# Kernel optimization log

Measured on AMD Instinct MI355X. Metric: run time of the kernel, lower is better.

The kernel has to match this reference:

```python
import jax, jax.numpy as jnp
import numpy as np


def _forgetting_attn(q, k, v, g):
    # q, k, v: [B, T, H, D]; g: [B, T, H] per-step log decay (log-space)
    scale = q.shape[-1] ** -0.5
    scores = jnp.einsum('bqhd,bkhd->bhqk', q, k) * scale  # [B,H,T,T]
    gc = jnp.cumsum(g, axis=1).transpose(0, 2, 1)  # [B,H,T]
    scores = scores + gc[:, :, :, None] - gc[:, :, None, :]
    T = q.shape[1]
    causal = jnp.tril(jnp.ones((T, T), dtype=bool))
    scores = jnp.where(causal, scores, -jnp.inf)
    probs = jax.nn.softmax(scores.astype(jnp.float32), axis=-1).astype(q.dtype)
    return jnp.einsum('bhqk,bkhd->bqhd', probs, v)  # [B,T,H,D]


def setup_inputs() -> dict:
    key = jax.random.key(0)
    ks = jax.random.split(key, 7)
    B, T, H = 1, 2048, 1024
    nh = 16
    s = 0.02
    return {
        'hidden_states': jax.random.normal(ks[0], (B, T, H), jnp.float32),
        'Wq': jax.random.normal(ks[1], (H, H), jnp.float32) * s,
        'Wk': jax.random.normal(ks[2], (H, H), jnp.float32) * s,
        'Wv': jax.random.normal(ks[3], (H, H), jnp.float32) * s,
        'Wf': jax.random.normal(ks[4], (nh, H), jnp.float32) * s,
        'bf': jnp.zeros((nh,), jnp.float32),
        'Wo': jax.random.normal(ks[5], (H, 2 * H), jnp.float32) * s,
    }


def reference(hidden_states, Wq, Wk, Wv, Wf, bf, Wo):
    B, T, H = hidden_states.shape
    nh = Wf.shape[0]
    d = H // nh
    q = (hidden_states @ Wq.T).reshape(B, T, nh, d)
    k = (hidden_states @ Wk.T).reshape(B, T, nh, d)
    v = (hidden_states @ Wv.T).reshape(B, T, nh, d)
    f = jax.nn.log_sigmoid((hidden_states @ Wf.T + bf).astype(jnp.float32))  # [B,T,nh]
    o_fwd = _forgetting_attn(q, k, v, f)
    flip = lambda x: jnp.flip(x, axis=1)
    o_bwd = flip(_forgetting_attn(flip(q), flip(k), flip(v), flip(f)))
    o = jnp.concatenate([o_fwd.reshape(B, T, H), o_bwd.reshape(B, T, H)], axis=-1)
    return o @ Wo.T
```

## Files before the change

kernel.cpp:

```cpp
#include <hip/hip_runtime.h>
#include <math.h>

#define T_SEQ 2048
#define HID   1024
#define NH    16
#define HD    64
#define NT    (T_SEQ / 64)

typedef __attribute__((ext_vector_type(8))) __bf16 bf16x8;
typedef __attribute__((ext_vector_type(4))) float  f32x4;
typedef __attribute__((ext_vector_type(8))) unsigned short u16x8;

#define GPTR(p) (const __attribute__((address_space(1))) void*)(p)
#define SPTR(p) (__attribute__((address_space(3))) void*)(p)

__device__ __forceinline__ unsigned short f2bf(float x) {
    unsigned u = __float_as_uint(x);
    u = (u + 0x7FFF + ((u >> 16) & 1)) >> 16;
    return (unsigned short)u;
}
__device__ __forceinline__ float bf2f(unsigned short u) {
    return __uint_as_float((unsigned)u << 16);
}

__global__ __launch_bounds__(256) void prep1(
    const float* __restrict__ hs,
    const float* __restrict__ Wq, const float* __restrict__ Wk,
    const float* __restrict__ Wv, const float* __restrict__ Wo,
    const float* __restrict__ Wf, const float* __restrict__ bfv,
    unsigned short* __restrict__ hsb, unsigned short* __restrict__ wqb,
    unsigned short* __restrict__ wkb, unsigned short* __restrict__ wvb,
    unsigned short* __restrict__ wob, float* __restrict__ f)
{
    const int y = blockIdx.y;
    if (y < 5) {
        const float* in; unsigned short* out; int n;
        switch (y) {
            case 0: in = hs; out = hsb; n = T_SEQ * HID; break;
            case 1: in = Wq; out = wqb; n = HID * HID;   break;
            case 2: in = Wk; out = wkb; n = HID * HID;   break;
            case 3: in = Wv; out = wvb; n = HID * HID;   break;
            default: in = Wo; out = wob; n = HID * 2 * HID; break;
        }
        const int stride = gridDim.x * blockDim.x;
        for (int i = blockIdx.x * blockDim.x + threadIdx.x; i < n / 4; i += stride) {
            float4 v = reinterpret_cast<const float4*>(in)[i];
            ushort4 r;
            r.x = f2bf(v.x); r.y = f2bf(v.y); r.z = f2bf(v.z); r.w = f2bf(v.w);
            reinterpret_cast<ushort4*>(out)[i] = r;
        }
    } else {
        const int t  = blockIdx.x;
        const int h  = threadIdx.x >> 4;
        const int sl = threadIdx.x & 15;
        const float4* hrow = reinterpret_cast<const float4*>(hs + (size_t)t * HID);
        const float4* wrow = reinterpret_cast<const float4*>(Wf + (size_t)h * HID);
        float s = 0.f;
        #pragma unroll
        for (int i = 0; i < 16; ++i) {
            float4 a = hrow[sl + i * 16];
            float4 b = wrow[sl + i * 16];
            s += a.x * b.x + a.y * b.y + a.z * b.z + a.w * b.w;
        }
        s += __shfl_xor(s, 1);
        s += __shfl_xor(s, 2);
        s += __shfl_xor(s, 4);
        s += __shfl_xor(s, 8);
        if (sl == 0) {
            float x = s + bfv[h];
            f[t * NH + h] = (x >= 0.f) ? -log1pf(expf(-x)) : (x - log1pf(expf(x)));
        }
    }
}

template<int FR>
__device__ __forceinline__ void stage_tile(const unsigned short* __restrict__ G, int K,
                                           int k0, unsigned short* lds, int tid, int w)
{
    #pragma unroll
    for (int j = 0; j < FR; ++j) {
        const int idxb = j * 4096 + tid * 16;
        const int row  = idxb >> 7;
        const int kbyt = idxb & 127;
        const int col  = (kbyt ^ ((row & 7) << 4)) >> 1;
        const int ldsh = (j * 4096 + w * 1024) >> 1;
        __builtin_amdgcn_global_load_lds(
            GPTR(G + (size_t)row * K + k0 + col), SPTR(lds + ldsh), 16, 0, 0);
    }
}

template<int BM, int BN, int EMODE>
__global__ __launch_bounds__(256) void gemm_mfma_bt(
    const unsigned short* __restrict__ A,
    const unsigned short* __restrict__ W0, const unsigned short* __restrict__ W1,
    const unsigned short* __restrict__ W2,
    float* __restrict__ C,
    unsigned short* __restrict__ qb, unsigned short* __restrict__ kb,
    unsigned short* __restrict__ vt,
    int M, int N, int K)
{
    const unsigned short* W = blockIdx.z == 0 ? W0 : (blockIdx.z == 1 ? W1 : W2);

    __shared__ unsigned short Als[2][BM * 64];
    __shared__ unsigned short Bls[2][BN * 64];

    const int gx  = gridDim.x;
    const int nwg = gx * gridDim.y;
    const int lin = blockIdx.y * gx + blockIdx.x;
    const int cpx = nwg >> 3;
    const int sw  = (lin & 7) * cpx + (lin >> 3);
    const int bx  = sw % gx;
    const int by  = sw / gx;

    const int tid = threadIdx.x;
    const int w   = tid >> 6;
    const int l   = tid & 63;
    const int bm  = by * BM;
    const int bn  = bx * BN;
    const int wm  = (w >> 1) * (BM / 2);
    const int wn  = (w & 1) * (BN / 2);
    constexpr int FM = BM / 32;
    constexpr int FN = BN / 32;

    f32x4 acc[FM][FN];
    #pragma unroll
    for (int m = 0; m < FM; ++m)
        #pragma unroll
        for (int n = 0; n < FN; ++n) acc[m][n] = (f32x4){0.f, 0.f, 0.f, 0.f};

    const int frow = l & 15;
    const int kgrp = (l >> 4) * 16;
    const int swz  = (l & 7) << 4;

    const unsigned short* Ag = A + (size_t)bm * K;
    const unsigned short* Wg = W + (size_t)bn * K;

    const int NIT = K >> 6;
    stage_tile<FM>(Ag, K, 0, Als[0], tid, w);
    stage_tile<FN>(Wg, K, 0, Bls[0], tid, w);
    __syncthreads();

    int cur = 0;
    for (int it = 0; it < NIT; ++it) {
        if (it + 1 < NIT) {
            stage_tile<FM>(Ag, K, (it + 1) * 64, Als[cur ^ 1], tid, w);
            stage_tile<FN>(Wg, K, (it + 1) * 64, Bls[cur ^ 1], tid, w);
        }
        const unsigned short* Ap = Als[cur];
        const unsigned short* Bp = Bls[cur];
        #pragma unroll
        for (int ks = 0; ks < 2; ++ks) {
            bf16x8 af[FM], bfr[FN];
            #pragma unroll
            for (int m = 0; m < FM; ++m) {
                const int off = (wm + m * 16 + frow) * 128 + ((ks * 64 + kgrp) ^ swz);
                af[m] = *reinterpret_cast<const bf16x8*>((const char*)Ap + off);
            }
            #pragma unroll
            for (int n = 0; n < FN; ++n) {
                const int off = (wn + n * 16 + frow) * 128 + ((ks * 64 + kgrp) ^ swz);
                bfr[n] = *reinterpret_cast<const bf16x8*>((const char*)Bp + off);
            }
            #pragma unroll
            for (int m = 0; m < FM; ++m)
                #pragma unroll
                for (int n = 0; n < FN; ++n)
                    acc[m][n] = __builtin_amdgcn_mfma_f32_16x16x32_bf16(
                        af[m], bfr[n], acc[m][n], 0, 0, 0);
        }
        __syncthreads();
        cur ^= 1;
    }

    const int r0 = (l >> 4) * 4;
    const int cc = l & 15;
    if (EMODE == 1) {
        #pragma unroll
        for (int m = 0; m < FM; ++m)
            #pragma unroll
            for (int n = 0; n < FN; ++n) {
                float* cp = C + (size_t)(bm + wm + m * 16 + r0) * N + bn + wn + n * 16 + cc;
                #pragma unroll
                for (int r = 0; r < 4; ++r) cp[(size_t)r * N] = acc[m][n][r];
            }
    } else {
        const int z = blockIdx.z;
        if (z == 0) {
            #pragma unroll
            for (int m = 0; m < FM; ++m) {
                const int t0 = bm + wm + m * 16 + r0;
                #pragma unroll
                for (int n = 0; n < FN; ++n) {
                    const int col = bn + wn + n * 16 + cc;
                    #pragma unroll
                    for (int r = 0; r < 4; ++r)
                        qb[(size_t)(t0 + r) * HID + col] = f2bf(acc[m][n][r] * 0.125f);
                }
            }
        } else if (z == 1) {
            #pragma unroll
            for (int m = 0; m < FM; ++m) {
                const int t0 = bm + wm + m * 16 + r0;
                #pragma unroll
                for (int n = 0; n < FN; ++n) {
                    const int col = bn + wn + n * 16 + cc;
                    const int hh  = col >> 6;
                    const int d   = col & 63;
                    #pragma unroll
                    for (int r = 0; r < 4; ++r)
                        kb[(size_t)hh * T_SEQ * HD + (size_t)(t0 + r) * HD + d] =
                            f2bf(acc[m][n][r]);
                }
            }
        } else {
            #pragma unroll
            for (int m = 0; m < FM; ++m) {
                const int t0 = bm + wm + m * 16 + r0;
                #pragma unroll
                for (int n = 0; n < FN; ++n) {
                    const int col = bn + wn + n * 16 + cc;
                    const int hh  = col >> 6;
                    const int d   = col & 63;
                    ushort4 pk;
                    pk.x = f2bf(acc[m][n][0]); pk.y = f2bf(acc[m][n][1]);
                    pk.z = f2bf(acc[m][n][2]); pk.w = f2bf(acc[m][n][3]);
                    *reinterpret_cast<ushort4*>(
                        vt + (size_t)hh * HD * T_SEQ + (size_t)d * T_SEQ + t0) = pk;
                }
            }
        }
    }
}

__global__ __launch_bounds__(256) void prep2(const float* __restrict__ f,
                                             float* __restrict__ gcf,
                                             float* __restrict__ gcb,
                                             const unsigned short* __restrict__ kb,
                                             float* __restrict__ knmax)
{
    const int bid = blockIdx.x;
    if (bid < 32) {
        const int h   = bid >> 1;
        const int rev = bid & 1;
        float* out = rev ? gcb : gcf;
        const int wv   = threadIdx.x >> 6;
        const int lane = threadIdx.x & 63;
        __shared__ float wtot[4];
        float vals[8];
        float run = 0.f;
        #pragma unroll
        for (int c = 0; c < 8; ++c) {
            const int p = wv * 512 + c * 64 + lane;
            const int t = rev ? (T_SEQ - 1 - p) : p;
            float x = f[t * NH + h];
            #pragma unroll
            for (int off = 1; off < 64; off <<= 1) {
                float y = __shfl_up(x, off);
                if (lane >= off) x += y;
            }
            vals[c] = run + x;
            run += __shfl(x, 63);
        }
        if (lane == 0) wtot[wv] = run;
        __syncthreads();
        float prefix = 0.f;
        #pragma unroll
        for (int i = 0; i < 4; ++i) prefix += (i < wv) ? wtot[i] : 0.f;
        #pragma unroll
        for (int c = 0; c < 8; ++c) {
            const int p = wv * 512 + c * 64 + lane;
            const int t = rev ? (T_SEQ - 1 - p) : p;
            out[t * NH + h] = vals[c] + prefix;
        }
    } else {
        const int h    = bid - 32;
        const int tid  = threadIdx.x;
        const int wv   = tid >> 6;
        const int lane = tid & 63;
        __shared__ float wmax[4];
        float mx = 0.f;
        for (int t = tid; t < T_SEQ; t += 256) {
            const u16x8* kr = reinterpret_cast<const u16x8*>(
                kb + (size_t)h * T_SEQ * HD + (size_t)t * HD);
            float s = 0.f;
            #pragma unroll
            for (int i = 0; i < 8; ++i) {
                u16x8 v8 = kr[i];
                #pragma unroll
                for (int j = 0; j < 8; ++j) { float x = bf2f(v8[j]); s += x * x; }
            }
            mx = fmaxf(mx, s);
        }
        #pragma unroll
        for (int off = 32; off > 0; off >>= 1) mx = fmaxf(mx, __shfl_xor(mx, off));
        if (lane == 0) wmax[wv] = mx;
        __syncthreads();
        if (tid == 0) {
            float m = fmaxf(fmaxf(wmax[0], wmax[1]), fmaxf(wmax[2], wmax[3]));
            knmax[h] = sqrtf(m);
        }
    }
}

__global__ __launch_bounds__(256) void attn_flash(
    const unsigned short* __restrict__ qb, const unsigned short* __restrict__ kg,
    const unsigned short* __restrict__ vg,
    const float* __restrict__ gcf, const float* __restrict__ gcb,
    const float* __restrict__ knmax,
    unsigned short* __restrict__ ocat)
{
    const int dir = blockIdx.z;
    const float* gc = dir ? gcb : gcf;
    const int h   = blockIdx.y;
    const int qt  = blockIdx.x;
    const int q0  = qt * 64;
    const int tid = threadIdx.x;
    const int w   = tid >> 6;
    const int l   = tid & 63;
    const int lm  = l & 15;
    const int lg  = l >> 4;
    const int swz = (l & 7) << 4;

    __shared__ unsigned short Kls[64 * 64];
    __shared__ unsigned short Vls[64 * 64];
    __shared__ unsigned short Pls[64 * 64];
    __shared__ float gks[64];
    __shared__ float qbs[64];

    const size_t kgbase = (size_t)h * T_SEQ * HD;
    const size_t vgbase = (size_t)h * HD * T_SEQ;

    const int qrow_a = q0 + 16 * w + lm;
    bf16x8 aq[2];
    aq[0] = *reinterpret_cast<const bf16x8*>(qb + (size_t)qrow_a * HID + h * HD + lg * 8);
    aq[1] = *reinterpret_cast<const bf16x8*>(qb + (size_t)qrow_a * HID + h * HD + 32 + lg * 8);
    float qn2 = 0.f;
    #pragma unroll
    for (int ks = 0; ks < 2; ++ks) {
        u16x8 uv = *reinterpret_cast<const u16x8*>(&aq[ks]);
        #pragma unroll
        for (int j = 0; j < 8; ++j) { float x = bf2f(uv[j]); qn2 += x * x; }
    }
    qn2 += __shfl_xor(qn2, 16);
    qn2 += __shfl_xor(qn2, 32);
    if (lg == 0) qbs[16 * w + lm] = sqrtf(qn2) * knmax[h];

    float gq_r[4];
    #pragma unroll
    for (int reg = 0; reg < 4; ++reg)
        gq_r[reg] = gc[(q0 + 16 * w + lg * 4 + reg) * NH + h];

    float mrun[4], lrun[4];
    #pragma unroll
    for (int reg = 0; reg < 4; ++reg) { mrun[reg] = -1e30f; lrun[reg] = 0.f; }
    f32x4 acc[4];
    #pragma unroll
    for (int db = 0; db < 4; ++db) acc[db] = (f32x4){0.f, 0.f, 0.f, 0.f};

    const int stp = dir ? 1 : -1;
    for (int kt = qt; kt >= 0 && kt < NT; kt += stp) {
        const int k0 = kt * 64;

        #pragma unroll
        for (int j = 0; j < 2; ++j) {
            const int idxb = j * 4096 + tid * 16;
            const int row  = idxb >> 7;
            const int kbyt = idxb & 127;
            const int scol = (kbyt ^ ((row & 7) << 4)) >> 1;
            const int ldsh = (j * 4096 + w * 1024) >> 1;
            __builtin_amdgcn_global_load_lds(
                GPTR(kg + kgbase + (size_t)(k0 + row) * HD + scol),
                SPTR(Kls + ldsh), 16, 0, 0);
            __builtin_amdgcn_global_load_lds(
                GPTR(vg + vgbase + (size_t)row * T_SEQ + k0 + scol),
                SPTR(Vls + ldsh), 16, 0, 0);
        }
        if (w == 0)
            __builtin_amdgcn_global_load_lds(
                GPTR(gc + (size_t)(k0 + l) * NH + h), SPTR(gks), 4, 0, 0);
        __syncthreads();

        f32x4 s[4];
        #pragma unroll
        for (int cb = 0; cb < 4; ++cb) {
            bf16x8 b0 = *reinterpret_cast<const bf16x8*>(
                (char*)Kls + (cb * 16 + lm) * 128 + ((lg * 16) ^ swz));
            bf16x8 b1 = *reinterpret_cast<const bf16x8*>(
                (char*)Kls + (cb * 16 + lm) * 128 + ((64 + lg * 16) ^ swz));
            f32x4 z = (f32x4){0.f, 0.f, 0.f, 0.f};
            z = __builtin_amdgcn_mfma_f32_16x16x32_bf16(aq[0], b0, z, 0, 0, 0);
            s[cb] = __builtin_amdgcn_mfma_f32_16x16x32_bf16(aq[1], b1, z, 0, 0, 0);
        }

        float gk_c[4];
        #pragma unroll
        for (int cb = 0; cb < 4; ++cb) gk_c[cb] = gks[cb * 16 + lm];
        float sv[4][4];
        const bool diag = (kt == qt);
        #pragma unroll
        for (int cb = 0; cb < 4; ++cb)
            #pragma unroll
            for (int reg = 0; reg < 4; ++reg) {
                float x = s[cb][reg] + gq_r[reg] - gk_c[cb];
                if (diag) {
                    const int c_loc = cb * 16 + lm;
                    const int r_loc = 16 * w + lg * 4 + reg;
                    const bool valid = dir ? (c_loc >= r_loc) : (c_loc <= r_loc);
                    x = valid ? x : -1e30f;
                }
                sv[cb][reg] = x;
            }

        float corr[4], mnew[4];
        #pragma unroll
        for (int reg = 0; reg < 4; ++reg) {
            float rm = fmaxf(fmaxf(sv[0][reg], sv[1][reg]), fmaxf(sv[2][reg], sv[3][reg]));
            rm = fmaxf(rm, __shfl_xor(rm, 1));
            rm = fmaxf(rm, __shfl_xor(rm, 2));
            rm = fmaxf(rm, __shfl_xor(rm, 4));
            rm = fmaxf(rm, __shfl_xor(rm, 8));
            mnew[reg] = fmaxf(mrun[reg], rm);
            corr[reg] = __expf(mrun[reg] - mnew[reg]);
            mrun[reg] = mnew[reg];
        }
        float psum[4] = {0.f, 0.f, 0.f, 0.f};
        #pragma unroll
        for (int cb = 0; cb < 4; ++cb)
            #pragma unroll
            for (int reg = 0; reg < 4; ++reg) {
                const float p = __expf(sv[cb][reg] - mnew[reg]);
                psum[reg] += p;
                const int r_loc = 16 * w + lg * 4 + reg;
                *reinterpret_cast<unsigned short*>(
                    (char*)Pls + r_loc * 128 + ((cb * 32 + lm * 2) ^ ((r_loc & 7) << 4))) = f2bf(p);
            }
        #pragma unroll
        for (int reg = 0; reg < 4; ++reg) {
            float ps = psum[reg];
            ps += __shfl_xor(ps, 1);
            ps += __shfl_xor(ps, 2);
            ps += __shfl_xor(ps, 4);
            ps += __shfl_xor(ps, 8);
            lrun[reg] = lrun[reg] * corr[reg] + ps;
        }
        #pragma unroll
        for (int db = 0; db < 4; ++db)
            #pragma unroll
            for (int reg = 0; reg < 4; ++reg) acc[db][reg] *= corr[reg];

        bf16x8 ap[2];
        #pragma unroll
        for (int ks = 0; ks < 2; ++ks)
            ap[ks] = *reinterpret_cast<const bf16x8*>(
                (char*)Pls + (16 * w + lm) * 128 + ((ks * 64 + lg * 16) ^ swz));
        #pragma unroll
        for (int db = 0; db < 4; ++db) {
            bf16x8 bv0 = *reinterpret_cast<const bf16x8*>(
                (char*)Vls + (db * 16 + lm) * 128 + ((lg * 16) ^ swz));
            bf16x8 bv1 = *reinterpret_cast<const bf16x8*>(
                (char*)Vls + (db * 16 + lm) * 128 + ((64 + lg * 16) ^ swz));
            acc[db] = __builtin_amdgcn_mfma_f32_16x16x32_bf16(ap[0], bv0, acc[db], 0, 0, 0);
            acc[db] = __builtin_amdgcn_mfma_f32_16x16x32_bf16(ap[1], bv1, acc[db], 0, 0, 0);
        }

        const int nkt = kt + stp;
        if (nkt >= 0 && nkt < NT) {
            const float gkedge = dir ? gc[(nkt * 64) * NH + h]
                                     : gc[(nkt * 64 + 63) * NH + h];
            int pred = 0;
            #pragma unroll
            for (int reg = 0; reg < 4; ++reg) {
                const float qbv = qbs[16 * w + lg * 4 + reg];
                pred |= (qbv + gq_r[reg] - gkedge) >= (mrun[reg] - 15.f);
            }
            if (!__syncthreads_or(pred)) break;
        }
    }

    float inv[4];
    #pragma unroll
    for (int reg = 0; reg < 4; ++reg) inv[reg] = 1.f / lrun[reg];
    #pragma unroll
    for (int db = 0; db < 4; ++db)
        #pragma unroll
        for (int reg = 0; reg < 4; ++reg) {
            const int row = q0 + 16 * w + lg * 4 + reg;
            const int col = db * 16 + lm;
            ocat[(size_t)row * (2 * HID) + dir * HID + h * HD + col] =
                f2bf(acc[db][reg] * inv[reg]);
        }
}

extern "C" void kernel_launch(void* const* d_in, const int* in_sizes, int n_in,
                              void* d_out, int out_size, void* d_ws, size_t ws_size,
                              hipStream_t stream)
{
    (void)in_sizes; (void)n_in; (void)out_size; (void)ws_size;
    const float* hs = (const float*)d_in[0];
    const float* Wq = (const float*)d_in[1];
    const float* Wk = (const float*)d_in[2];
    const float* Wv = (const float*)d_in[3];
    const float* Wf = (const float*)d_in[4];
    const float* bf = (const float*)d_in[5];
    const float* Wo = (const float*)d_in[6];
    float* out = (float*)d_out;

    float* ws    = (float*)d_ws;
    float* f     = ws;
    float* gcf   = f   + (size_t)T_SEQ * NH;
    float* gcb   = gcf + (size_t)T_SEQ * NH;
    float* knmax = gcb + (size_t)T_SEQ * NH;
    unsigned short* hsb  = (unsigned short*)(knmax + 64);
    unsigned short* wqb  = hsb + (size_t)T_SEQ * HID;
    unsigned short* wkb  = wqb + (size_t)HID * HID;
    unsigned short* wvb  = wkb + (size_t)HID * HID;
    unsigned short* wob  = wvb + (size_t)HID * HID;
    unsigned short* qb   = wob + (size_t)HID * 2 * HID;
    unsigned short* kb   = qb  + (size_t)T_SEQ * HID;
    unsigned short* vt   = kb  + (size_t)T_SEQ * HID;
    unsigned short* ocat = vt  + (size_t)T_SEQ * HID;

    prep1<<<dim3(2048, 6), 256, 0, stream>>>(
        hs, Wq, Wk, Wv, Wo, Wf, bf, hsb, wqb, wkb, wvb, wob, f);

    gemm_mfma_bt<128, 64, 0><<<dim3(HID / 64, T_SEQ / 128, 3), 256, 0, stream>>>(
        hsb, wqb, wkb, wvb, nullptr, qb, kb, vt, T_SEQ, HID, HID);

    prep2<<<48, 256, 0, stream>>>(f, gcf, gcb, kb, knmax);

    attn_flash<<<dim3(NT, NH, 2), 256, 0, stream>>>(qb, kb, vt, gcf, gcb, knmax, ocat);

    gemm_mfma_bt<64, 64, 1><<<dim3(HID / 64, T_SEQ / 64, 1), 256, 0, stream>>>(
        ocat, wob, nullptr, nullptr, out, nullptr, nullptr, nullptr,
        T_SEQ, HID, 2 * HID);
}
```

Baseline: 93.35 us.

## Load K/V tiles directly from global memory and use per-wave early exit

```diff
diff --git a/kernel.cpp b/kernel.cpp
--- a/kernel.cpp
+++ b/kernel.cpp
@@ -101,6 +101,9 @@
 {
     const unsigned short* W = blockIdx.z == 0 ? W0 : (blockIdx.z == 1 ? W1 : W2);
 
+    constexpr int FM = BM / 32;
+    constexpr int FN = BN / 32;
+
     __shared__ unsigned short Als[2][BM * 64];
     __shared__ unsigned short Bls[2][BN * 64];
 
@@ -119,8 +122,6 @@
     const int bn  = bx * BN;
     const int wm  = (w >> 1) * (BM / 2);
     const int wn  = (w & 1) * (BN / 2);
-    constexpr int FM = BM / 32;
-    constexpr int FN = BN / 32;
 
     f32x4 acc[FM][FN];
     #pragma unroll
@@ -321,14 +322,11 @@
     const int lg  = l >> 4;
     const int swz = (l & 7) << 4;
 
-    __shared__ unsigned short Kls[64 * 64];
-    __shared__ unsigned short Vls[64 * 64];
     __shared__ unsigned short Pls[64 * 64];
-    __shared__ float gks[64];
     __shared__ float qbs[64];
 
-    const size_t kgbase = (size_t)h * T_SEQ * HD;
-    const size_t vgbase = (size_t)h * HD * T_SEQ;
+    const unsigned short* kh = kg + (size_t)h * T_SEQ * HD;
+    const unsigned short* vh = vg + (size_t)h * HD * T_SEQ;
 
     const int qrow_a = q0 + 16 * w + lm;
     bf16x8 aq[2];
@@ -361,32 +359,12 @@
     for (int kt = qt; kt >= 0 && kt < NT; kt += stp) {
         const int k0 = kt * 64;
 
-        #pragma unroll
-        for (int j = 0; j < 2; ++j) {
-            const int idxb = j * 4096 + tid * 16;
-            const int row  = idxb >> 7;
-            const int kbyt = idxb & 127;
-            const int scol = (kbyt ^ ((row & 7) << 4)) >> 1;
-            const int ldsh = (j * 4096 + w * 1024) >> 1;
-            __builtin_amdgcn_global_load_lds(
-                GPTR(kg + kgbase + (size_t)(k0 + row) * HD + scol),
-                SPTR(Kls + ldsh), 16, 0, 0);
-            __builtin_amdgcn_global_load_lds(
-                GPTR(vg + vgbase + (size_t)row * T_SEQ + k0 + scol),
-                SPTR(Vls + ldsh), 16, 0, 0);
-        }
-        if (w == 0)
-            __builtin_amdgcn_global_load_lds(
-                GPTR(gc + (size_t)(k0 + l) * NH + h), SPTR(gks), 4, 0, 0);
-        __syncthreads();
-
         f32x4 s[4];
         #pragma unroll
         for (int cb = 0; cb < 4; ++cb) {
-            bf16x8 b0 = *reinterpret_cast<const bf16x8*>(
-                (char*)Kls + (cb * 16 + lm) * 128 + ((lg * 16) ^ swz));
-            bf16x8 b1 = *reinterpret_cast<const bf16x8*>(
-                (char*)Kls + (cb * 16 + lm) * 128 + ((64 + lg * 16) ^ swz));
+            const unsigned short* kr = kh + (size_t)(k0 + cb * 16 + lm) * HD + lg * 8;
+            bf16x8 b0 = *reinterpret_cast<const bf16x8*>(kr);
+            bf16x8 b1 = *reinterpret_cast<const bf16x8*>(kr + 32);
             f32x4 z = (f32x4){0.f, 0.f, 0.f, 0.f};
             z = __builtin_amdgcn_mfma_f32_16x16x32_bf16(aq[0], b0, z, 0, 0, 0);
             s[cb] = __builtin_amdgcn_mfma_f32_16x16x32_bf16(aq[1], b1, z, 0, 0, 0);
@@ -394,7 +372,7 @@
 
         float gk_c[4];
         #pragma unroll
-        for (int cb = 0; cb < 4; ++cb) gk_c[cb] = gks[cb * 16 + lm];
+        for (int cb = 0; cb < 4; ++cb) gk_c[cb] = gc[(k0 + cb * 16 + lm) * NH + h];
         float sv[4][4];
         const bool diag = (kt == qt);
         #pragma unroll
@@ -455,10 +433,9 @@
                 (char*)Pls + (16 * w + lm) * 128 + ((ks * 64 + lg * 16) ^ swz));
         #pragma unroll
         for (int db = 0; db < 4; ++db) {
-            bf16x8 bv0 = *reinterpret_cast<const bf16x8*>(
-                (char*)Vls + (db * 16 + lm) * 128 + ((lg * 16) ^ swz));
-            bf16x8 bv1 = *reinterpret_cast<const bf16x8*>(
-                (char*)Vls + (db * 16 + lm) * 128 + ((64 + lg * 16) ^ swz));
+            const unsigned short* vr = vh + (size_t)(db * 16 + lm) * T_SEQ + k0 + lg * 8;
+            bf16x8 bv0 = *reinterpret_cast<const bf16x8*>(vr);
+            bf16x8 bv1 = *reinterpret_cast<const bf16x8*>(vr + 32);
             acc[db] = __builtin_amdgcn_mfma_f32_16x16x32_bf16(ap[0], bv0, acc[db], 0, 0, 0);
             acc[db] = __builtin_amdgcn_mfma_f32_16x16x32_bf16(ap[1], bv1, acc[db], 0, 0, 0);
         }
@@ -473,7 +450,7 @@
                 const float qbv = qbs[16 * w + lg * 4 + reg];
                 pred |= (qbv + gq_r[reg] - gkedge) >= (mrun[reg] - 15.f);
             }
-            if (!__syncthreads_or(pred)) break;
+            if (!__any(pred)) break;
         }
     }
 
```

After: 101.4 us. 8.6% more time.
